# Kernel tuning notes

Hardware: AMD Instinct MI355X
Metric: run time of the kernel (lower is better)

The kernel has to match this reference:

```python
import jax, jax.numpy as jnp
import numpy as np

B, K, L, D = 64, 49, 200, 36  # batch, ref time points, seq len, n variables
INIT_TIME, PRIOR_HOURS = 0.0, 48.0


def setup_inputs() -> dict:
    key = jax.random.key(0)
    ks = jax.random.split(key, 9)
    X = jax.random.normal(ks[0], (B, L, D), dtype=jnp.float32)
    T = jax.random.uniform(ks[1], (B, L, D), dtype=jnp.float32) * PRIOR_HOURS
    M = (jax.random.uniform(ks[2], (B, L, D)) > 0.5).astype(jnp.float32)
    PD = jax.random.uniform(ks[3], (B, L, D), dtype=jnp.float32)
    # learned params per ALNNLayer.build (glorot-like small init)
    def glorot(k, shape):
        fan = sum(shape)
        lim = jnp.sqrt(6.0 / fan)
        return jax.random.uniform(k, shape, jnp.float32, -lim, lim)
    alpha = glorot(ks[4], (K, 1, 1))
    w_v = glorot(ks[5], (K, L, D))
    w_t = glorot(ks[6], (K, L, D, 4))
    b_v = glorot(ks[7], (K, 1, D))
    b_t = glorot(ks[8], (K, L, D, 1))
    return {"X": X, "T": T, "M": M, "PD": PD,
            "alpha": alpha, "w_v": w_v, "w_t": w_t, "b_v": b_v, "b_t": b_t}


def reference(X, T, M, PD, alpha, w_v, w_t, b_v, b_t):
    k = alpha.shape[0]
    # reference time points [K,1,1]
    ref_time = jnp.linspace(INIT_TIME, PRIOR_HOURS, k, dtype=jnp.float32).reshape(k, 1, 1)
    # broadcast [B,1,L,D] against [K,1,1] -> [B,K,L,D]
    dist = jnp.abs(T[:, None, :, :] - ref_time)           # type_distance == 'abs'
    kernel = jnp.exp(-jax.nn.relu(alpha) * dist)          # [B,K,L,D]
    intensity = jax.nn.relu(X[:, None, :, :] * kernel)    # [B,K,L,D]
    shp = intensity.shape
    # 4-channel concat on a trailing axis: [B,K,L,D,4]
    c = jnp.stack([
        jnp.broadcast_to(X[:, None, :, :], shp),
        intensity,
        jnp.broadcast_to(M[:, None, :, :], shp),
        jnp.broadcast_to(PD[:, None, :, :], shp),
    ], axis=-1)
    # stage 1: reduce_sum(w_t*c + b_t, axis=4); b_t broadcast over 4 channels -> contributes 4*b_t
    s1 = jax.nn.relu(jnp.einsum('bklds,klds->bkld', c, w_t) + 4.0 * b_t[..., 0])
    # stage 2: reduce_sum(w_v*s1 + b_v, axis=2); b_v [K,1,D] broadcast over L -> contributes L*b_v
    n_l = s1.shape[2]
    out = jax.nn.relu(jnp.einsum('bkld,kld->bkd', s1, w_v) + jnp.float32(n_l) * b_v[:, 0, :])
    return out  # [B,K,D]
```

## Files before the change

### kernel.cpp

```cpp
#include <hip/hip_runtime.h>

#define NB 64
#define NK 49
#define NL 200
#define ND 36
#define LD (NL*ND)

#define AT_FLOATS  (LD*NB*4)
#define WPK_FLOATS (LD*NK*6)
#define WPK_OFF   AT_FLOATS
#define WS_PACK_BYTES ((size_t)(AT_FLOATS + WPK_FLOATS) * 4)

#define LOG2E 1.44269504088896f

#if __has_builtin(__builtin_amdgcn_exp2f)
#define EXP2F(x) __builtin_amdgcn_exp2f(x)
#else
#define EXP2F(x) __expf((x) * 0.6931471805599453f)
#endif

__global__ __launch_bounds__(256) void alnn_pack(
    const float* __restrict__ X, const float* __restrict__ T,
    const float* __restrict__ M, const float* __restrict__ PD,
    const float* __restrict__ w_v, const float4* __restrict__ w_t,
    const float* __restrict__ b_t, float* __restrict__ ws)
{
    __shared__ float tile[9440];
    const int bid = blockIdx.x, t = threadIdx.x;

    if (bid < 225) {
        const int ld0 = bid * 32;
        const int ld = t & 31, bq = t >> 5;
        const float* src[4] = {X, T, M, PD};
        #pragma unroll
        for (int a = 0; a < 4; a++) {
            const float* A = src[a];
            for (int b = bq; b < 64; b += 8)
                tile[(a * 64 + b) * 33 + ld] = A[(size_t)b * LD + ld0 + ld];
        }
        __syncthreads();
        float4* At4 = (float4*)ws;
        const int b = t & 63, ldq = t >> 6;
        #pragma unroll
        for (int r = 0; r < 8; r++) {
            const int l = ldq * 8 + r;
            float4 v;
            v.x = tile[(0 * 64 + b) * 33 + l];
            v.y = tile[(1 * 64 + b) * 33 + l];
            v.z = tile[(2 * 64 + b) * 33 + l];
            v.w = tile[(3 * 64 + b) * 33 + l];
            At4[(size_t)(ld0 + l) * 64 + b] = v;
        }
    } else {
        const int ld0 = (bid - 225) * 32;
        const int ld = t & 31, kq = t >> 5;
        for (int k = kq; k < NK; k += 8) {
            const float4 wt = w_t[(size_t)k * LD + ld0 + ld];
            const float  bt = b_t[(size_t)k * LD + ld0 + ld];
            const float  wv = w_v[(size_t)k * LD + ld0 + ld];
            float* w = tile + ld * 295 + k * 6;
            w[0] = wt.x; w[1] = wt.y; w[2] = wt.z; w[3] = wt.w;
            w[4] = 4.0f * bt; w[5] = wv;
        }
        __syncthreads();
        float* Wpk = ws + WPK_OFF + (size_t)ld0 * 294;
        for (int i = t; i < 32 * 294; i += 256) {
            const int l = i / 294, r = i - l * 294;
            Wpk[i] = tile[l * 295 + r];
        }
    }
}

__global__ __launch_bounds__(512) void alnn_main2(
    const float* __restrict__ ws_ro, const float* __restrict__ alpha,
    const float* __restrict__ b_v, float* __restrict__ out)
{
    __shared__ float red[8 * 7 * 64];

    const int orig = blockIdx.x;
    const int xcd  = orig & 7, slot = orig >> 3;
    const int base = (xcd < 4) ? xcd * 32 : 128 + (xcd - 4) * 31;
    const int job  = base + slot;

    const int d  = job / 7, ks = job - (job / 7) * 7;
    const int t  = threadIdx.x;
    const int b  = t & 63;
    const int w  = __builtin_amdgcn_readfirstlane(t >> 6);
    const int k0 = ks * 7;

    const float4* At4 = (const float4*)ws_ro;
    const float*  Wpk = ws_ro + WPK_OFF;

    float arn[7], rk[7];
    #pragma unroll
    for (int kk = 0; kk < 7; kk++) {
        arn[kk] = -fmaxf(alpha[k0 + kk], 0.0f) * LOG2E;
        rk[kk]  = (float)(k0 + kk);
    }

    float acc[7] = {0, 0, 0, 0, 0, 0, 0};

    const int lbeg = w * 25;
    #pragma unroll 5
    for (int ll = 0; ll < 25; ll++) {
        const int ld = (lbeg + ll) * ND + d;
        const float4 av = At4[(size_t)ld * 64 + b];
        const float xp = fmaxf(av.x, 0.0f);
        const float* wr = Wpk + (size_t)ld * 294 + k0 * 6;
        #pragma unroll
        for (int kk = 0; kk < 7; kk++) {
            const float dist = fabsf(av.y - rk[kk]);
            const float e    = EXP2F(arn[kk] * dist);
            float s = fmaf(wr[kk*6+0], av.x,
                      fmaf(wr[kk*6+1], xp * e,
                      fmaf(wr[kk*6+2], av.z,
                      fmaf(wr[kk*6+3], av.w, wr[kk*6+4]))));
            acc[kk] = fmaf(wr[kk*6+5], fmaxf(s, 0.0f), acc[kk]);
        }
    }

    #pragma unroll
    for (int kk = 0; kk < 7; kk++)
        red[(w * 7 + kk) * 64 + b] = acc[kk];
    __syncthreads();

    if (w < 7) {
        const int kk = w, k = k0 + kk;
        float sum = 0.0f;
        #pragma unroll
        for (int ww = 0; ww < 8; ww++)
            sum += red[(ww * 7 + kk) * 64 + b];
        out[((size_t)b * NK + k) * ND + d] =
            fmaxf(sum + 200.0f * b_v[k * ND + d], 0.0f);
    }
}

__global__ __launch_bounds__(256) void alnn_fused_kernel(
    const float* __restrict__ X, const float* __restrict__ T,
    const float* __restrict__ M, const float* __restrict__ PD,
    const float* __restrict__ alpha, const float* __restrict__ w_v,
    const float4* __restrict__ w_t, const float* __restrict__ b_v,
    const float* __restrict__ b_t, float* __restrict__ out)
{
    const int bk = blockIdx.x;
    const int k  = bk % NK;
    const int b  = bk / NK;
    const int t  = threadIdx.x;

    __shared__ float part[7][ND];

    const float alpha_k = fmaxf(alpha[k], 0.0f);
    const float refk    = (float)k;

    if (t < 7 * ND) {
        const int d = t % ND;
        const int j = t / ND;
        const float*  Xp  = X   + (size_t)b * LD + d;
        const float*  Tp  = T   + (size_t)b * LD + d;
        const float*  Mp  = M   + (size_t)b * LD + d;
        const float*  Pp  = PD  + (size_t)b * LD + d;
        const float*  wvp = w_v + (size_t)k * LD + d;
        const float*  btp = b_t + (size_t)k * LD + d;
        const float4* wtp = w_t + (size_t)k * LD + d;

        float acc = 0.0f;
        for (int l = j; l < NL; l += 7) {
            const int o = l * ND;
            const float x  = Xp[o];
            const float tt = Tp[o];
            const float m  = Mp[o];
            const float pd = Pp[o];
            const float4 wv4 = wtp[o];
            const float bt = btp[o];
            const float dist  = fabsf(tt - refk);
            const float e     = __expf(-alpha_k * dist);
            const float inten = fmaxf(x * e, 0.0f);
            float s = fmaf(wv4.x, x, fmaf(wv4.y, inten, fmaf(wv4.z, m, fmaf(wv4.w, pd, 4.0f * bt))));
            s = fmaxf(s, 0.0f);
            acc = fmaf(wvp[o], s, acc);
        }
        part[j][d] = acc;
    }
    __syncthreads();

    if (t < ND) {
        float sum = 0.0f;
        #pragma unroll
        for (int j = 0; j < 7; ++j) sum += part[j][t];
        sum += (float)NL * b_v[k * ND + t];
        out[(size_t)bk * ND + t] = fmaxf(sum, 0.0f);
    }
}

extern "C" void kernel_launch(void* const* d_in, const int* in_sizes, int n_in,
                              void* d_out, int out_size, void* d_ws, size_t ws_size,
                              hipStream_t stream) {
    const float* X     = (const float*)d_in[0];
    const float* T     = (const float*)d_in[1];
    const float* M     = (const float*)d_in[2];
    const float* PD    = (const float*)d_in[3];
    const float* alpha = (const float*)d_in[4];
    const float* w_v   = (const float*)d_in[5];
    const float* w_t   = (const float*)d_in[6];
    const float* b_v   = (const float*)d_in[7];
    const float* b_t   = (const float*)d_in[8];
    float* out = (float*)d_out;
    float* ws  = (float*)d_ws;

    if (ws_size >= WS_PACK_BYTES) {
        alnn_pack<<<450, 256, 0, stream>>>(X, T, M, PD, w_v, (const float4*)w_t, b_t, ws);
        alnn_main2<<<252, 512, 0, stream>>>(ws, alpha, b_v, out);
    } else {
        alnn_fused_kernel<<<NB * NK, 256, 0, stream>>>(
            X, T, M, PD, alpha, w_v, (const float4*)w_t, b_v, b_t, out);
    }
}
```

Measured before the change: 30.76 us.

## Drop weight packing pass; read weights directly in main kernel with 1024 threads

Removes the weight-repacking half of the pack kernel, so the main kernel reads w_t, b_t and w_v straight from their original layouts, broadcast across the 64 batch lanes. The main kernel grows to 1024 threads (16 waves) with the L dimension split 13/12 per wave and a 16-way shared reduction. This saves writing and re-reading the packed weight buffer. In exchange, weight loads become scattered per-k reads with larger strides, and the bigger blocks may lower occupancy.

```diff
diff --git a/kernel.cpp b/kernel.cpp
--- a/kernel.cpp
+++ b/kernel.cpp
@@ -7,9 +7,7 @@
 #define LD (NL*ND)
 
 #define AT_FLOATS  (LD*NB*4)
-#define WPK_FLOATS (LD*NK*6)
-#define WPK_OFF   AT_FLOATS
-#define WS_PACK_BYTES ((size_t)(AT_FLOATS + WPK_FLOATS) * 4)
+#define WS_MIN_BYTES ((size_t)AT_FLOATS * 4)
 
 #define LOG2E 1.44269504088896f
 
@@ -19,63 +17,45 @@
 #define EXP2F(x) __expf((x) * 0.6931471805599453f)
 #endif
 
-__global__ __launch_bounds__(256) void alnn_pack(
+__global__ __launch_bounds__(256) void alnn_pack_act(
     const float* __restrict__ X, const float* __restrict__ T,
     const float* __restrict__ M, const float* __restrict__ PD,
-    const float* __restrict__ w_v, const float4* __restrict__ w_t,
-    const float* __restrict__ b_t, float* __restrict__ ws)
+    float* __restrict__ ws)
 {
-    __shared__ float tile[9440];
+    __shared__ float tile[4 * 64 * 33];
     const int bid = blockIdx.x, t = threadIdx.x;
-
-    if (bid < 225) {
-        const int ld0 = bid * 32;
-        const int ld = t & 31, bq = t >> 5;
-        const float* src[4] = {X, T, M, PD};
-        #pragma unroll
-        for (int a = 0; a < 4; a++) {
-            const float* A = src[a];
-            for (int b = bq; b < 64; b += 8)
-                tile[(a * 64 + b) * 33 + ld] = A[(size_t)b * LD + ld0 + ld];
-        }
-        __syncthreads();
-        float4* At4 = (float4*)ws;
-        const int b = t & 63, ldq = t >> 6;
-        #pragma unroll
-        for (int r = 0; r < 8; r++) {
-            const int l = ldq * 8 + r;
-            float4 v;
-            v.x = tile[(0 * 64 + b) * 33 + l];
-            v.y = tile[(1 * 64 + b) * 33 + l];
-            v.z = tile[(2 * 64 + b) * 33 + l];
-            v.w = tile[(3 * 64 + b) * 33 + l];
-            At4[(size_t)(ld0 + l) * 64 + b] = v;
-        }
-    } else {
-        const int ld0 = (bid - 225) * 32;
-        const int ld = t & 31, kq = t >> 5;
-        for (int k = kq; k < NK; k += 8) {
-            const float4 wt = w_t[(size_t)k * LD + ld0 + ld];
-            const float  bt = b_t[(size_t)k * LD + ld0 + ld];
-            const float  wv = w_v[(size_t)k * LD + ld0 + ld];
-            float* w = tile + ld * 295 + k * 6;
-            w[0] = wt.x; w[1] = wt.y; w[2] = wt.z; w[3] = wt.w;
-            w[4] = 4.0f * bt; w[5] = wv;
-        }
-        __syncthreads();
-        float* Wpk = ws + WPK_OFF + (size_t)ld0 * 294;
-        for (int i = t; i < 32 * 294; i += 256) {
-            const int l = i / 294, r = i - l * 294;
-            Wpk[i] = tile[l * 295 + r];
-        }
-    }
-}
-
-__global__ __launch_bounds__(512) void alnn_main2(
+    const int ld0 = bid * 32;
+    const int ld = t & 31, bq = t >> 5;
+    const float* src[4] = {X, T, M, PD};
+    #pragma unroll
+    for (int a = 0; a < 4; a++) {
+        const float* A = src[a];
+        #pragma unroll
+        for (int b = bq; b < 64; b += 8)
+            tile[(a * 64 + b) * 33 + ld] = A[(size_t)b * LD + ld0 + ld];
+    }
+    __syncthreads();
+    float4* At4 = (float4*)ws;
+    const int b = t & 63, ldq = t >> 6;
+    #pragma unroll
+    for (int r = 0; r < 8; r++) {
+        const int l = ldq * 8 + r;
+        float4 v;
+        v.x = tile[(0 * 64 + b) * 33 + l];
+        v.y = tile[(1 * 64 + b) * 33 + l];
+        v.z = tile[(2 * 64 + b) * 33 + l];
+        v.w = tile[(3 * 64 + b) * 33 + l];
+        At4[(size_t)(ld0 + l) * 64 + b] = v;
+    }
+}
+
+__global__ __launch_bounds__(1024) void alnn_main3(
     const float* __restrict__ ws_ro, const float* __restrict__ alpha,
-    const float* __restrict__ b_v, float* __restrict__ out)
+    const float4* __restrict__ w_t, const float* __restrict__ b_t,
+    const float* __restrict__ w_v, const float* __restrict__ b_v,
+    float* __restrict__ out)
 {
-    __shared__ float red[8 * 7 * 64];
+    __shared__ float red[16 * 7 * 64];
 
     const int orig = blockIdx.x;
     const int xcd  = orig & 7, slot = orig >> 3;
@@ -89,7 +69,6 @@
     const int k0 = ks * 7;
 
     const float4* At4 = (const float4*)ws_ro;
-    const float*  Wpk = ws_ro + WPK_OFF;
 
     float arn[7], rk[7];
     #pragma unroll
@@ -100,22 +79,27 @@
 
     float acc[7] = {0, 0, 0, 0, 0, 0, 0};
 
-    const int lbeg = w * 25;
-    #pragma unroll 5
-    for (int ll = 0; ll < 25; ll++) {
-        const int ld = (lbeg + ll) * ND + d;
+    const int len  = (w < 8) ? 13 : 12;
+    const int lbeg = (w < 8) ? 13 * w : 104 + 12 * (w - 8);
+
+    for (int ll = 0; ll < len; ll++) {
+        const int l  = lbeg + ll;
+        const int ld = l * ND + d;
         const float4 av = At4[(size_t)ld * 64 + b];
         const float xp = fmaxf(av.x, 0.0f);
-        const float* wr = Wpk + (size_t)ld * 294 + k0 * 6;
         #pragma unroll
         for (int kk = 0; kk < 7; kk++) {
+            const size_t wi = (size_t)(k0 + kk) * LD + ld;
+            const float4 wt = w_t[wi];
+            const float  bt = b_t[wi];
+            const float  wv = w_v[wi];
             const float dist = fabsf(av.y - rk[kk]);
             const float e    = EXP2F(arn[kk] * dist);
-            float s = fmaf(wr[kk*6+0], av.x,
-                      fmaf(wr[kk*6+1], xp * e,
-                      fmaf(wr[kk*6+2], av.z,
-                      fmaf(wr[kk*6+3], av.w, wr[kk*6+4]))));
-            acc[kk] = fmaf(wr[kk*6+5], fmaxf(s, 0.0f), acc[kk]);
+            float s = fmaf(wt.x, av.x,
+                      fmaf(wt.y, xp * e,
+                      fmaf(wt.z, av.z,
+                      fmaf(wt.w, av.w, 4.0f * bt))));
+            acc[kk] = fmaf(wv, fmaxf(s, 0.0f), acc[kk]);
         }
     }
 
@@ -128,7 +112,7 @@
         const int kk = w, k = k0 + kk;
         float sum = 0.0f;
         #pragma unroll
-        for (int ww = 0; ww < 8; ww++)
+        for (int ww = 0; ww < 16; ww++)
             sum += red[(ww * 7 + kk) * 64 + b];
         out[((size_t)b * NK + k) * ND + d] =
             fmaxf(sum + 200.0f * b_v[k * ND + d], 0.0f);
@@ -207,9 +191,9 @@
     float* out = (float*)d_out;
     float* ws  = (float*)d_ws;
 
-    if (ws_size >= WS_PACK_BYTES) {
-        alnn_pack<<<450, 256, 0, stream>>>(X, T, M, PD, w_v, (const float4*)w_t, b_t, ws);
-        alnn_main2<<<252, 512, 0, stream>>>(ws, alpha, b_v, out);
+    if (ws_size >= WS_MIN_BYTES) {
+        alnn_pack_act<<<225, 256, 0, stream>>>(X, T, M, PD, ws);
+        alnn_main3<<<252, 1024, 0, stream>>>(ws, alpha, (const float4*)w_t, b_t, w_v, b_v, out);
     } else {
         alnn_fused_kernel<<<NB * NK, 256, 0, stream>>>(
             X, T, M, PD, alpha, w_v, (const float4*)w_t, b_v, b_t, out);
```

Result: slower. 47.41 us (+54.1%).
